# Kernel optimization log

Hardware: AMD Instinct MI355X
Metric: run time of the kernel (lower is better)

## Reference

```python
import jax, jax.numpy as jnp
import numpy as np

B, L, H = 32, 512, 1024
Q = 128
VA_H = 256

def setup_inputs() -> dict:
    key = jax.random.key(0)
    ks = jax.random.split(key, 12)
    hidden_states = jax.random.normal(ks[0], (B, L, H), dtype=jnp.float32)
    # Build valid inclusive spans: start in [2, L-16), length in [0, 8)
    asp_s = jax.random.randint(ks[1], (B, Q), 2, L - 16)
    asp_e = asp_s + jax.random.randint(ks[2], (B, Q), 0, 8)
    opi_s = jax.random.randint(ks[3], (B, Q), 2, L - 16)
    opi_e = opi_s + jax.random.randint(ks[4], (B, Q), 0, 8)
    null = jax.random.uniform(ks[5], (B, Q)) < 0.1
    asp_s = jnp.where(null, 0, asp_s)
    quad_spans = jnp.stack([asp_s, asp_e, opi_s, opi_e], axis=-1).astype(jnp.int64)
    quad_mask = (jax.random.uniform(ks[6], (B, Q)) > 0.3).astype(jnp.float32)
    # MLP params (torch Linear: y = x @ W.T + b), kaiming-ish scale
    def lin(k, out_d, in_d):
        return jax.random.normal(k, (out_d, in_d), dtype=jnp.float32) / np.sqrt(in_d)
    W1 = lin(ks[7], VA_H, 3 * H); b1 = jnp.zeros((VA_H,), jnp.float32)
    W2 = lin(ks[8], VA_H // 2, VA_H); b2 = jnp.zeros((VA_H // 2,), jnp.float32)
    W3 = lin(ks[9], 2, VA_H // 2); b3 = jnp.zeros((2,), jnp.float32)
    return {"hidden_states": hidden_states, "quad_spans": quad_spans,
            "quad_mask": quad_mask, "W1": W1, "b1": b1, "W2": W2, "b2": b2,
            "W3": W3, "b3": b3}

def _pool_spans(hidden_states, s, e):
    # hidden_states: [B,L,H]; s,e: [B,Q] inclusive indices
    pos = jnp.arange(hidden_states.shape[1])  # [L]
    valid = (s >= 2) & (e >= s)               # [B,Q]
    m = (pos[None, None, :] >= s[..., None]) & (pos[None, None, :] <= e[..., None])
    m = (m & valid[..., None]).astype(hidden_states.dtype)  # [B,Q,L]
    cnt = jnp.maximum(m.sum(-1, keepdims=True), 1.0)        # [B,Q,1]
    mean = jnp.einsum('bql,blh->bqh', m, hidden_states) / cnt
    sep = hidden_states[:, 1:2, :]                           # [B,1,H] fallback
    return jnp.where(valid[..., None], mean, sep)

def reference(hidden_states, quad_spans, quad_mask, W1, b1, W2, b2, W3, b3):
    h_asp = _pool_spans(hidden_states, quad_spans[..., 0], quad_spans[..., 1])
    h_opi = _pool_spans(hidden_states, quad_spans[..., 2], quad_spans[..., 3])
    h_pair = jnp.concatenate([h_asp, h_opi, h_asp * h_opi], axis=-1)  # [B,Q,3H]
    x = jax.nn.gelu(h_pair @ W1.T + b1, approximate=False)  # torch GELU = erf
    x = jax.nn.gelu(x @ W2.T + b2, approximate=False)
    va = jax.nn.sigmoid(x @ W3.T + b3) * 8.0 + 1.0          # [B,Q,2] in [1,9]
    # Invalid pairs stay zero, matching the torch loop's skipped entries
    return va * (quad_mask >= 0.5).astype(va.dtype)[..., None]
```

## Files before the change

kernel.cpp:

```cpp
#include <hip/hip_runtime.h>
#include <hip/hip_bf16.h>
#include <math.h>

typedef __bf16 bf16x8 __attribute__((ext_vector_type(8)));
typedef float f32x4 __attribute__((ext_vector_type(4)));

__device__ __forceinline__ unsigned short f2bf(float x) {
    union { float f; unsigned int u; } v; v.f = x;
    unsigned int r = v.u + 0x7fffu + ((v.u >> 16) & 1u);
    return (unsigned short)(r >> 16);
}
__device__ __forceinline__ float gelu_exact(float v) {
    return 0.5f * v * (1.0f + erff(v * 0.70710678118654752f));
}

template<int N>
__device__ __forceinline__ void pool_sum(const float4* __restrict__ base, int s, int tid, float4& out) {
    float4 v[N];
#pragma unroll
    for (int t = 0; t < N; ++t) v[t] = base[(s + t) * 256 + tid];
    float x = 0.f, y = 0.f, z = 0.f, w = 0.f;
#pragma unroll
    for (int t = 0; t < N; ++t) { x += v[t].x; y += v[t].y; z += v[t].z; w += v[t].w; }
    const float inv = 1.0f / (float)N;
    out.x = x * inv; out.y = y * inv; out.z = z * inv; out.w = w * inv;
}

__device__ __forceinline__ void pool_dispatch(const float4* __restrict__ base, int s, int len, int tid, float4& out) {
    switch (len) {
        case 1: pool_sum<1>(base, s, tid, out); break;
        case 2: pool_sum<2>(base, s, tid, out); break;
        case 3: pool_sum<3>(base, s, tid, out); break;
        case 4: pool_sum<4>(base, s, tid, out); break;
        case 5: pool_sum<5>(base, s, tid, out); break;
        case 6: pool_sum<6>(base, s, tid, out); break;
        case 7: pool_sum<7>(base, s, tid, out); break;
        default: pool_sum<8>(base, s, tid, out); break;
    }
}

__global__ __launch_bounds__(256) void prep_kernel(const float* __restrict__ hs,
                                                   const int* __restrict__ spans,
                                                   const float* __restrict__ W1,
                                                   const float* __restrict__ W2,
                                                   unsigned short* __restrict__ hp,
                                                   unsigned short* __restrict__ w1b,
                                                   unsigned short* __restrict__ w2b) {
    const int blk = blockIdx.x;
    const int tid = threadIdx.x;

    if (blk >= 4096) {
        if (blk < 4864) {
            const int i = (blk - 4096) * 256 + tid;
            float4 f = ((const float4*)W1)[i];
            ushort4 u;
            u.x = f2bf(f.x); u.y = f2bf(f.y); u.z = f2bf(f.z); u.w = f2bf(f.w);
            ((ushort4*)w1b)[i] = u;
        } else {
            const int i = (blk - 4864) * 256 + tid;
            float4 f = ((const float4*)W2)[i];
            ushort4 u;
            u.x = f2bf(f.x); u.y = f2bf(f.y); u.z = f2bf(f.z); u.w = f2bf(f.w);
            ((ushort4*)w2b)[i] = u;
        }
        return;
    }

    const int pair = blk;
    const int b = pair >> 7;

    const bool is64 = (spans[1] == 0);
    int s_a, e_a, s_o, e_o;
    if (is64) {
        s_a = spans[(pair * 4 + 0) * 2]; e_a = spans[(pair * 4 + 1) * 2];
        s_o = spans[(pair * 4 + 2) * 2]; e_o = spans[(pair * 4 + 3) * 2];
    } else {
        s_a = spans[pair * 4 + 0]; e_a = spans[pair * 4 + 1];
        s_o = spans[pair * 4 + 2]; e_o = spans[pair * 4 + 3];
    }

    if (!(s_a >= 2 && e_a >= s_a)) { s_a = 1; e_a = 1; }
    if (!(s_o >= 2 && e_o >= s_o)) { s_o = 1; e_o = 1; }
    const int lenA = e_a - s_a + 1;
    const int lenO = e_o - s_o + 1;

    const float4* base = (const float4*)hs + (size_t)b * 512 * 256;

    float4 A, O;
    pool_dispatch(base, s_a, lenA, tid, A);
    pool_dispatch(base, s_o, lenO, tid, O);

    unsigned short* row = hp + (size_t)pair * 3072;
    const int d = tid * 4;
    ushort4 pa, po, pp;
    pa.x = f2bf(A.x); pa.y = f2bf(A.y); pa.z = f2bf(A.z); pa.w = f2bf(A.w);
    po.x = f2bf(O.x); po.y = f2bf(O.y); po.z = f2bf(O.z); po.w = f2bf(O.w);
    pp.x = f2bf(A.x * O.x); pp.y = f2bf(A.y * O.y);
    pp.z = f2bf(A.z * O.z); pp.w = f2bf(A.w * O.w);
    *(ushort4*)(row + d) = pa;
    *(ushort4*)(row + 1024 + d) = po;
    *(ushort4*)(row + 2048 + d) = pp;
}

__global__ __launch_bounds__(256, 2) void gemm1_gelu(const unsigned short* __restrict__ A,
                                                     const unsigned short* __restrict__ Bw,
                                                     const float* __restrict__ b1,
                                                     unsigned short* __restrict__ x1) {
    __shared__ __align__(16) unsigned short As[2 * 32 * 192];
    __shared__ __align__(16) unsigned short Bs[2 * 64 * 192];

    const int tid = threadIdx.x;
    const int lane = tid & 63;
    const int wid = tid >> 6;
    const int quad = lane >> 4;
    const int l16 = lane & 15;

    const int id = blockIdx.x;
    const int xcd = id & 7;
    const int sub = id >> 3;
    const int m0 = (xcd * 16 + (sub >> 2)) * 32;
    const int n0 = (sub & 3) * 64;

    const unsigned short* Aptr[3];
#pragma unroll
    for (int p = 0; p < 3; ++p) {
        const int s = p * 256 + tid;
        const int row = s / 24;
        const int c = s - row * 24;
        const int lch = (c & 24) | ((c & 7) ^ (row & 7));
        Aptr[p] = A + (size_t)(m0 + row) * 3072 + lch * 8;
    }
    const unsigned short* Bptr[6];
#pragma unroll
    for (int p = 0; p < 6; ++p) {
        const int s = p * 256 + tid;
        const int row = s / 24;
        const int c = s - row * 24;
        const int lch = (c & 24) | ((c & 7) ^ (row & 7));
        Bptr[p] = Bw + (size_t)(n0 + row) * 3072 + lch * 8;
    }

    int aoff[2][6], boff[6];
#pragma unroll
    for (int h = 0; h < 6; ++h) {
        const int c = h * 4 + quad;
#pragma unroll
        for (int mh = 0; mh < 2; ++mh) {
            const int row = mh * 16 + l16;
            const int pc = (c & 24) | ((c & 7) ^ (row & 7));
            aoff[mh][h] = row * 192 + pc * 8;
        }
        const int brow = wid * 16 + l16;
        const int pcb = (c & 24) | ((c & 7) ^ (brow & 7));
        boff[h] = brow * 192 + pcb * 8;
    }

    f32x4 acc[2] = {};

#pragma unroll
    for (int p = 0; p < 3; ++p)
        __builtin_amdgcn_global_load_lds(
            (const __attribute__((address_space(1))) void*)Aptr[p],
            (__attribute__((address_space(3))) void*)(&As[(p * 256 + tid) * 8]), 16, 0, 0);
#pragma unroll
    for (int p = 0; p < 6; ++p)
        __builtin_amdgcn_global_load_lds(
            (const __attribute__((address_space(1))) void*)Bptr[p],
            (__attribute__((address_space(3))) void*)(&Bs[(p * 256 + tid) * 8]), 16, 0, 0);

    for (int it = 0; it < 16; ++it) {
        const int cur = it & 1;
        __syncthreads();
        if (it + 1 < 16) {
            const int nxt = cur ^ 1;
            const int kadv = (it + 1) * 192;
#pragma unroll
            for (int p = 0; p < 3; ++p)
                __builtin_amdgcn_global_load_lds(
                    (const __attribute__((address_space(1))) void*)(Aptr[p] + kadv),
                    (__attribute__((address_space(3))) void*)(&As[nxt * 6144 + (p * 256 + tid) * 8]), 16, 0, 0);
#pragma unroll
            for (int p = 0; p < 6; ++p)
                __builtin_amdgcn_global_load_lds(
                    (const __attribute__((address_space(1))) void*)(Bptr[p] + kadv),
                    (__attribute__((address_space(3))) void*)(&Bs[nxt * 12288 + (p * 256 + tid) * 8]), 16, 0, 0);
        }
#pragma unroll
        for (int h = 0; h < 6; ++h) {
            bf16x8 b = *(const bf16x8*)&Bs[cur * 12288 + boff[h]];
#pragma unroll
            for (int mh = 0; mh < 2; ++mh) {
                bf16x8 a = *(const bf16x8*)&As[cur * 6144 + aoff[mh][h]];
                acc[mh] = __builtin_amdgcn_mfma_f32_16x16x32_bf16(a, b, acc[mh], 0, 0, 0);
            }
        }
    }

    const int n = n0 + wid * 16 + l16;
    const float bn = b1[n];
#pragma unroll
    for (int mh = 0; mh < 2; ++mh) {
#pragma unroll
        for (int rr = 0; rr < 4; ++rr) {
            const int m = m0 + mh * 16 + quad * 4 + rr;
            x1[(size_t)m * 256 + n] = f2bf(gelu_exact(acc[mh][rr] + bn));
        }
    }
}

__global__ __launch_bounds__(256) void mlp2_head(const unsigned short* __restrict__ x1,
                                                 const unsigned short* __restrict__ w2b,
                                                 const float* __restrict__ b2,
                                                 const float* __restrict__ W3,
                                                 const float* __restrict__ b3,
                                                 const float* __restrict__ mask,
                                                 float* __restrict__ out) {
    __shared__ __align__(16) unsigned char smem[98304];
    unsigned short* Xs = (unsigned short*)smem;
    unsigned short* Ws = (unsigned short*)(smem + 16384);
    float*          X2 = (float*)(smem + 81920);

    const int tid = threadIdx.x;
    const int lane = tid & 63;
    const int wid = tid >> 6;
    const int quad = lane >> 4;
    const int l16 = lane & 15;
    const int wM = (wid >> 1) * 16;
    const int wN = (wid & 1) * 64;
    const int m0 = blockIdx.x * 32;

#pragma unroll
    for (int p = 0; p < 4; ++p) {
        const int s = p * 256 + tid;
        const int row = s >> 5;
        const int c = s & 31;
        const int lch = (c & 24) | ((c & 7) ^ (row & 7));
        __builtin_amdgcn_global_load_lds(
            (const __attribute__((address_space(1))) void*)(x1 + (size_t)(m0 + row) * 256 + lch * 8),
            (__attribute__((address_space(3))) void*)(&Xs[s * 8]), 16, 0, 0);
    }
#pragma unroll
    for (int p = 0; p < 16; ++p) {
        const int s = p * 256 + tid;
        const int row = s >> 5;
        const int c = s & 31;
        const int lch = (c & 24) | ((c & 7) ^ (row & 7));
        __builtin_amdgcn_global_load_lds(
            (const __attribute__((address_space(1))) void*)(w2b + (size_t)row * 256 + lch * 8),
            (__attribute__((address_space(3))) void*)(&Ws[s * 8]), 16, 0, 0);
    }
    __syncthreads();

    f32x4 acc[4] = {};
#pragma unroll
    for (int h = 0; h < 8; ++h) {
        const int c = h * 4 + quad;
        const int rowa = wM + l16;
        const int pca = (c & 24) | ((c & 7) ^ (rowa & 7));
        bf16x8 a = *(const bf16x8*)&Xs[rowa * 256 + pca * 8];
#pragma unroll
        for (int ni = 0; ni < 4; ++ni) {
            const int rowb = wN + ni * 16 + l16;
            const int pcb = (c & 24) | ((c & 7) ^ (rowb & 7));
            bf16x8 b = *(const bf16x8*)&Ws[rowb * 256 + pcb * 8];
            acc[ni] = __builtin_amdgcn_mfma_f32_16x16x32_bf16(a, b, acc[ni], 0, 0, 0);
        }
    }

#pragma unroll
    for (int ni = 0; ni < 4; ++ni) {
        const int n = wN + ni * 16 + l16;
        const float bn = b2[n];
#pragma unroll
        for (int rr = 0; rr < 4; ++rr) {
            const int m = wM + quad * 4 + rr;
            X2[m * 128 + n] = gelu_exact(acc[ni][rr] + bn);
        }
    }
    __syncthreads();

    const int p = tid >> 3;
    const int cc = (tid & 7) * 16;
    float a0 = 0.f, a1 = 0.f;
#pragma unroll
    for (int j = 0; j < 16; ++j) {
        const float xv = X2[p * 128 + cc + j];
        a0 += xv * W3[cc + j];
        a1 += xv * W3[128 + cc + j];
    }
    a0 += __shfl_xor(a0, 1); a0 += __shfl_xor(a0, 2); a0 += __shfl_xor(a0, 4);
    a1 += __shfl_xor(a1, 1); a1 += __shfl_xor(a1, 2); a1 += __shfl_xor(a1, 4);
    if ((tid & 7) == 0) {
        const int pair = m0 + p;
        const float mk = (mask[pair] >= 0.5f) ? 1.0f : 0.0f;
        out[pair * 2 + 0] = ((1.0f / (1.0f + expf(-(a0 + b3[0])))) * 8.0f + 1.0f) * mk;
        out[pair * 2 + 1] = ((1.0f / (1.0f + expf(-(a1 + b3[1])))) * 8.0f + 1.0f) * mk;
    }
}

extern "C" void kernel_launch(void* const* d_in, const int* in_sizes, int n_in,
                              void* d_out, int out_size, void* d_ws, size_t ws_size,
                              hipStream_t stream) {
    const float* hs   = (const float*)d_in[0];
    const int*   spans= (const int*)d_in[1];
    const float* mask = (const float*)d_in[2];
    const float* W1   = (const float*)d_in[3];
    const float* b1   = (const float*)d_in[4];
    const float* W2   = (const float*)d_in[5];
    const float* b2   = (const float*)d_in[6];
    const float* W3   = (const float*)d_in[7];
    const float* b3   = (const float*)d_in[8];
    float* out = (float*)d_out;

    unsigned short* hp  = (unsigned short*)d_ws;
    unsigned short* w1b = (unsigned short*)((char*)d_ws + 25165824);
    unsigned short* x1  = (unsigned short*)((char*)d_ws + 26738688);
    unsigned short* w2b = (unsigned short*)((char*)d_ws + 28835840);

    prep_kernel<<<dim3(4896), dim3(256), 0, stream>>>(hs, spans, W1, W2, hp, w1b, w2b);
    gemm1_gelu<<<dim3(512), dim3(256), 0, stream>>>(hp, w1b, b1, x1);
    mlp2_head<<<dim3(128), dim3(256), 0, stream>>>(x1, w2b, b2, W3, b3, mask, out);
}
```

Measured before the change: 145.3 us.

## Fuse prep, GEMM1 and MLP head into one cooperative persistent kernel

```diff
diff --git a/kernel.cpp b/kernel.cpp
--- a/kernel.cpp
+++ b/kernel.cpp
@@ -1,6 +1,9 @@
 #include <hip/hip_runtime.h>
+#include <hip/hip_cooperative_groups.h>
 #include <hip/hip_bf16.h>
 #include <math.h>
+
+namespace cg = cooperative_groups;
 
 typedef __bf16 bf16x8 __attribute__((ext_vector_type(8)));
 typedef float f32x4 __attribute__((ext_vector_type(4)));
@@ -25,7 +28,6 @@
     const float inv = 1.0f / (float)N;
     out.x = x * inv; out.y = y * inv; out.z = z * inv; out.w = w * inv;
 }
-
 __device__ __forceinline__ void pool_dispatch(const float4* __restrict__ base, int s, int len, int tid, float4& out) {
     switch (len) {
         case 1: pool_sum<1>(base, s, tid, out); break;
@@ -39,262 +41,248 @@
     }
 }
 
-__global__ __launch_bounds__(256) void prep_kernel(const float* __restrict__ hs,
-                                                   const int* __restrict__ spans,
-                                                   const float* __restrict__ W1,
-                                                   const float* __restrict__ W2,
-                                                   unsigned short* __restrict__ hp,
-                                                   unsigned short* __restrict__ w1b,
-                                                   unsigned short* __restrict__ w2b) {
-    const int blk = blockIdx.x;
+__global__ __launch_bounds__(256, 2) void fused_all(
+        const float* __restrict__ hs, const int* __restrict__ spans,
+        const float* __restrict__ W1, const float* __restrict__ b1,
+        const float* __restrict__ W2, const float* __restrict__ b2,
+        const float* __restrict__ W3, const float* __restrict__ b3,
+        const float* __restrict__ mask, float* __restrict__ out,
+        unsigned short* __restrict__ hp, unsigned short* __restrict__ w1b,
+        unsigned short* __restrict__ x1, unsigned short* __restrict__ w2b) {
+    __shared__ __align__(16) unsigned char smem[73728];
+    unsigned short* As = (unsigned short*)smem;
+    unsigned short* Bs = (unsigned short*)(smem + 24576);
+    unsigned short* Ws = (unsigned short*)smem;
+    float*      scratch = (float*)(smem + 65536);
+
     const int tid = threadIdx.x;
-
-    if (blk >= 4096) {
-        if (blk < 4864) {
-            const int i = (blk - 4096) * 256 + tid;
-            float4 f = ((const float4*)W1)[i];
-            ushort4 u;
-            u.x = f2bf(f.x); u.y = f2bf(f.y); u.z = f2bf(f.z); u.w = f2bf(f.w);
-            ((ushort4*)w1b)[i] = u;
-        } else {
-            const int i = (blk - 4864) * 256 + tid;
-            float4 f = ((const float4*)W2)[i];
-            ushort4 u;
-            u.x = f2bf(f.x); u.y = f2bf(f.y); u.z = f2bf(f.z); u.w = f2bf(f.w);
-            ((ushort4*)w2b)[i] = u;
-        }
-        return;
-    }
-
-    const int pair = blk;
-    const int b = pair >> 7;
-
-    const bool is64 = (spans[1] == 0);
-    int s_a, e_a, s_o, e_o;
-    if (is64) {
-        s_a = spans[(pair * 4 + 0) * 2]; e_a = spans[(pair * 4 + 1) * 2];
-        s_o = spans[(pair * 4 + 2) * 2]; e_o = spans[(pair * 4 + 3) * 2];
-    } else {
-        s_a = spans[pair * 4 + 0]; e_a = spans[pair * 4 + 1];
-        s_o = spans[pair * 4 + 2]; e_o = spans[pair * 4 + 3];
-    }
-
-    if (!(s_a >= 2 && e_a >= s_a)) { s_a = 1; e_a = 1; }
-    if (!(s_o >= 2 && e_o >= s_o)) { s_o = 1; e_o = 1; }
-    const int lenA = e_a - s_a + 1;
-    const int lenO = e_o - s_o + 1;
-
-    const float4* base = (const float4*)hs + (size_t)b * 512 * 256;
-
-    float4 A, O;
-    pool_dispatch(base, s_a, lenA, tid, A);
-    pool_dispatch(base, s_o, lenO, tid, O);
-
-    unsigned short* row = hp + (size_t)pair * 3072;
-    const int d = tid * 4;
-    ushort4 pa, po, pp;
-    pa.x = f2bf(A.x); pa.y = f2bf(A.y); pa.z = f2bf(A.z); pa.w = f2bf(A.w);
-    po.x = f2bf(O.x); po.y = f2bf(O.y); po.z = f2bf(O.z); po.w = f2bf(O.w);
-    pp.x = f2bf(A.x * O.x); pp.y = f2bf(A.y * O.y);
-    pp.z = f2bf(A.z * O.z); pp.w = f2bf(A.w * O.w);
-    *(ushort4*)(row + d) = pa;
-    *(ushort4*)(row + 1024 + d) = po;
-    *(ushort4*)(row + 2048 + d) = pp;
-}
-
-__global__ __launch_bounds__(256, 2) void gemm1_gelu(const unsigned short* __restrict__ A,
-                                                     const unsigned short* __restrict__ Bw,
-                                                     const float* __restrict__ b1,
-                                                     unsigned short* __restrict__ x1) {
-    __shared__ __align__(16) unsigned short As[2 * 32 * 192];
-    __shared__ __align__(16) unsigned short Bs[2 * 64 * 192];
-
-    const int tid = threadIdx.x;
+    const int id = blockIdx.x;
     const int lane = tid & 63;
     const int wid = tid >> 6;
     const int quad = lane >> 4;
     const int l16 = lane & 15;
 
-    const int id = blockIdx.x;
     const int xcd = id & 7;
     const int sub = id >> 3;
-    const int m0 = (xcd * 16 + (sub >> 2)) * 32;
-    const int n0 = (sub & 3) * 64;
-
-    const unsigned short* Aptr[3];
-#pragma unroll
-    for (int p = 0; p < 3; ++p) {
-        const int s = p * 256 + tid;
-        const int row = s / 24;
-        const int c = s - row * 24;
-        const int lch = (c & 24) | ((c & 7) ^ (row & 7));
-        Aptr[p] = A + (size_t)(m0 + row) * 3072 + lch * 8;
+    const int mp = xcd * 16 + (sub >> 2);
+    const int jj = sub & 3;
+    const int m0 = mp * 32;
+    const int n0 = jj * 64;
+
+    {
+        const bool is64 = (spans[1] == 0);
+        for (int pp = 0; pp < 8; ++pp) {
+            const int pair = m0 + jj * 8 + pp;
+            const int b = pair >> 7;
+            int s_a, e_a, s_o, e_o;
+            if (is64) {
+                s_a = spans[(pair * 4 + 0) * 2]; e_a = spans[(pair * 4 + 1) * 2];
+                s_o = spans[(pair * 4 + 2) * 2]; e_o = spans[(pair * 4 + 3) * 2];
+            } else {
+                s_a = spans[pair * 4 + 0]; e_a = spans[pair * 4 + 1];
+                s_o = spans[pair * 4 + 2]; e_o = spans[pair * 4 + 3];
+            }
+            if (!(s_a >= 2 && e_a >= s_a)) { s_a = 1; e_a = 1; }
+            if (!(s_o >= 2 && e_o >= s_o)) { s_o = 1; e_o = 1; }
+            const float4* base = (const float4*)hs + (size_t)b * 512 * 256;
+            float4 A, O;
+            pool_dispatch(base, s_a, e_a - s_a + 1, tid, A);
+            pool_dispatch(base, s_o, e_o - s_o + 1, tid, O);
+
+            unsigned short* row = hp + (size_t)pair * 3072;
+            const int d = tid * 4;
+            ushort4 pa, po, pq;
+            pa.x = f2bf(A.x); pa.y = f2bf(A.y); pa.z = f2bf(A.z); pa.w = f2bf(A.w);
+            po.x = f2bf(O.x); po.y = f2bf(O.y); po.z = f2bf(O.z); po.w = f2bf(O.w);
+            pq.x = f2bf(A.x * O.x); pq.y = f2bf(A.y * O.y);
+            pq.z = f2bf(A.z * O.z); pq.w = f2bf(A.w * O.w);
+            *(ushort4*)(row + d) = pa;
+            *(ushort4*)(row + 1024 + d) = po;
+            *(ushort4*)(row + 2048 + d) = pq;
+        }
+        const int g = id * 256 + tid;
+        {
+            float4 f = ((const float4*)W1)[g];
+            ushort4 u;
+            u.x = f2bf(f.x); u.y = f2bf(f.y); u.z = f2bf(f.z); u.w = f2bf(f.w);
+            ((ushort4*)w1b)[g] = u;
+            const int g2 = g + 131072;
+            if (g2 < 196608) {
+                float4 f2 = ((const float4*)W1)[g2];
+                ushort4 u2;
+                u2.x = f2bf(f2.x); u2.y = f2bf(f2.y); u2.z = f2bf(f2.z); u2.w = f2bf(f2.w);
+                ((ushort4*)w1b)[g2] = u2;
+            }
+        }
+        if (g < 8192) {
+            float4 f = ((const float4*)W2)[g];
+            ushort4 u;
+            u.x = f2bf(f.x); u.y = f2bf(f.y); u.z = f2bf(f.z); u.w = f2bf(f.w);
+            ((ushort4*)w2b)[g] = u;
+        }
     }
-    const unsigned short* Bptr[6];
-#pragma unroll
-    for (int p = 0; p < 6; ++p) {
-        const int s = p * 256 + tid;
-        const int row = s / 24;
-        const int c = s - row * 24;
-        const int lch = (c & 24) | ((c & 7) ^ (row & 7));
-        Bptr[p] = Bw + (size_t)(n0 + row) * 3072 + lch * 8;
+    __threadfence();
+    cg::this_grid().sync();
+
+    {
+        const unsigned short* Ap = hp;
+        const unsigned short* Bw = w1b;
+
+        const unsigned short* Aptr[3];
+#pragma unroll
+        for (int p = 0; p < 3; ++p) {
+            const int s = p * 256 + tid;
+            const int row = s / 24;
+            const int c = s - row * 24;
+            const int lch = (c & 24) | ((c & 7) ^ (row & 7));
+            Aptr[p] = Ap + (size_t)(m0 + row) * 3072 + lch * 8;
+        }
+        const unsigned short* Bptr[6];
+#pragma unroll
+        for (int p = 0; p < 6; ++p) {
+            const int s = p * 256 + tid;
+            const int row = s / 24;
+            const int c = s - row * 24;
+            const int lch = (c & 24) | ((c & 7) ^ (row & 7));
+            Bptr[p] = Bw + (size_t)(n0 + row) * 3072 + lch * 8;
+        }
+
+        int aoff[2][6], boff[6];
+#pragma unroll
+        for (int h = 0; h < 6; ++h) {
+            const int c = h * 4 + quad;
+#pragma unroll
+            for (int mh = 0; mh < 2; ++mh) {
+                const int row = mh * 16 + l16;
+                const int pc = (c & 24) | ((c & 7) ^ (row & 7));
+                aoff[mh][h] = row * 192 + pc * 8;
+            }
+            const int brow = wid * 16 + l16;
+            const int pcb = (c & 24) | ((c & 7) ^ (brow & 7));
+            boff[h] = brow * 192 + pcb * 8;
+        }
+
+        f32x4 acc[2] = {};
+
+#pragma unroll
+        for (int p = 0; p < 3; ++p)
+            __builtin_amdgcn_global_load_lds(
+                (const __attribute__((address_space(1))) void*)Aptr[p],
+                (__attribute__((address_space(3))) void*)(&As[(p * 256 + tid) * 8]), 16, 0, 0);
+#pragma unroll
+        for (int p = 0; p < 6; ++p)
+            __builtin_amdgcn_global_load_lds(
+                (const __attribute__((address_space(1))) void*)Bptr[p],
+                (__attribute__((address_space(3))) void*)(&Bs[(p * 256 + tid) * 8]), 16, 0, 0);
+
+        for (int it = 0; it < 16; ++it) {
+            const int cur = it & 1;
+            __syncthreads();
+            if (it + 1 < 16) {
+                const int nxt = cur ^ 1;
+                const int kadv = (it + 1) * 192;
+#pragma unroll
+                for (int p = 0; p < 3; ++p)
+                    __builtin_amdgcn_global_load_lds(
+                        (const __attribute__((address_space(1))) void*)(Aptr[p] + kadv),
+                        (__attribute__((address_space(3))) void*)(&As[nxt * 6144 + (p * 256 + tid) * 8]), 16, 0, 0);
+#pragma unroll
+                for (int p = 0; p < 6; ++p)
+                    __builtin_amdgcn_global_load_lds(
+                        (const __attribute__((address_space(1))) void*)(Bptr[p] + kadv),
+                        (__attribute__((address_space(3))) void*)(&Bs[nxt * 12288 + (p * 256 + tid) * 8]), 16, 0, 0);
+            }
+#pragma unroll
+            for (int h = 0; h < 6; ++h) {
+                bf16x8 bfr = *(const bf16x8*)&Bs[cur * 12288 + boff[h]];
+#pragma unroll
+                for (int mh = 0; mh < 2; ++mh) {
+                    bf16x8 afr = *(const bf16x8*)&As[cur * 6144 + aoff[mh][h]];
+                    acc[mh] = __builtin_amdgcn_mfma_f32_16x16x32_bf16(afr, bfr, acc[mh], 0, 0, 0);
+                }
+            }
+        }
+
+        const int n = n0 + wid * 16 + l16;
+        const float bn = b1[n];
+#pragma unroll
+        for (int mh = 0; mh < 2; ++mh) {
+#pragma unroll
+            for (int rr = 0; rr < 4; ++rr) {
+                const int m = m0 + mh * 16 + quad * 4 + rr;
+                x1[(size_t)m * 256 + n] = f2bf(gelu_exact(acc[mh][rr] + bn));
+            }
+        }
     }
-
-    int aoff[2][6], boff[6];
-#pragma unroll
-    for (int h = 0; h < 6; ++h) {
-        const int c = h * 4 + quad;
-#pragma unroll
-        for (int mh = 0; mh < 2; ++mh) {
-            const int row = mh * 16 + l16;
-            const int pc = (c & 24) | ((c & 7) ^ (row & 7));
-            aoff[mh][h] = row * 192 + pc * 8;
-        }
-        const int brow = wid * 16 + l16;
-        const int pcb = (c & 24) | ((c & 7) ^ (brow & 7));
-        boff[h] = brow * 192 + pcb * 8;
-    }
-
-    f32x4 acc[2] = {};
-
-#pragma unroll
-    for (int p = 0; p < 3; ++p)
-        __builtin_amdgcn_global_load_lds(
-            (const __attribute__((address_space(1))) void*)Aptr[p],
-            (__attribute__((address_space(3))) void*)(&As[(p * 256 + tid) * 8]), 16, 0, 0);
-#pragma unroll
-    for (int p = 0; p < 6; ++p)
-        __builtin_amdgcn_global_load_lds(
-            (const __attribute__((address_space(1))) void*)Bptr[p],
-            (__attribute__((address_space(3))) void*)(&Bs[(p * 256 + tid) * 8]), 16, 0, 0);
-
-    for (int it = 0; it < 16; ++it) {
-        const int cur = it & 1;
+    __threadfence();
+    cg::this_grid().sync();
+
+    if (id >= 128) return;
+    {
+        const int m0c = id * 32;
+        const int wM = (wid >> 1) * 16;
+        const int wN = (wid & 1) * 64;
+        const int half = wid & 1;
+
+#pragma unroll
+        for (int p = 0; p < 16; ++p) {
+            const int s = p * 256 + tid;
+            const int row = s >> 5;
+            const int c = s & 31;
+            const int lch = (c & 24) | ((c & 7) ^ (row & 7));
+            __builtin_amdgcn_global_load_lds(
+                (const __attribute__((address_space(1))) void*)(w2b + (size_t)row * 256 + lch * 8),
+                (__attribute__((address_space(3))) void*)(&Ws[s * 8]), 16, 0, 0);
+        }
         __syncthreads();
-        if (it + 1 < 16) {
-            const int nxt = cur ^ 1;
-            const int kadv = (it + 1) * 192;
-#pragma unroll
-            for (int p = 0; p < 3; ++p)
-                __builtin_amdgcn_global_load_lds(
-                    (const __attribute__((address_space(1))) void*)(Aptr[p] + kadv),
-                    (__attribute__((address_space(3))) void*)(&As[nxt * 6144 + (p * 256 + tid) * 8]), 16, 0, 0);
-#pragma unroll
-            for (int p = 0; p < 6; ++p)
-                __builtin_amdgcn_global_load_lds(
-                    (const __attribute__((address_space(1))) void*)(Bptr[p] + kadv),
-                    (__attribute__((address_space(3))) void*)(&Bs[nxt * 12288 + (p * 256 + tid) * 8]), 16, 0, 0);
-        }
-#pragma unroll
-        for (int h = 0; h < 6; ++h) {
-            bf16x8 b = *(const bf16x8*)&Bs[cur * 12288 + boff[h]];
-#pragma unroll
-            for (int mh = 0; mh < 2; ++mh) {
-                bf16x8 a = *(const bf16x8*)&As[cur * 6144 + aoff[mh][h]];
-                acc[mh] = __builtin_amdgcn_mfma_f32_16x16x32_bf16(a, b, acc[mh], 0, 0, 0);
-            }
-        }
-    }
-
-    const int n = n0 + wid * 16 + l16;
-    const float bn = b1[n];
-#pragma unroll
-    for (int mh = 0; mh < 2; ++mh) {
+
+        f32x4 acc2[4] = {};
+        const unsigned short* arow = x1 + (size_t)(m0c + wM + l16) * 256;
+#pragma unroll
+        for (int h = 0; h < 8; ++h) {
+            bf16x8 afr = *(const bf16x8*)(arow + h * 32 + quad * 8);
+#pragma unroll
+            for (int ni = 0; ni < 4; ++ni) {
+                const int rowb = wN + ni * 16 + l16;
+                const int c = h * 4 + quad;
+                const int pcb = (c & 24) | ((c & 7) ^ (rowb & 7));
+                bf16x8 bfr = *(const bf16x8*)&Ws[rowb * 256 + pcb * 8];
+                acc2[ni] = __builtin_amdgcn_mfma_f32_16x16x32_bf16(afr, bfr, acc2[ni], 0, 0, 0);
+            }
+        }
+
+        float b2v[4], w30[4], w31[4];
+#pragma unroll
+        for (int ni = 0; ni < 4; ++ni) {
+            const int col = wN + ni * 16 + l16;
+            b2v[ni] = b2[col]; w30[ni] = W3[col]; w31[ni] = W3[128 + col];
+        }
 #pragma unroll
         for (int rr = 0; rr < 4; ++rr) {
-            const int m = m0 + mh * 16 + quad * 4 + rr;
-            x1[(size_t)m * 256 + n] = f2bf(gelu_exact(acc[mh][rr] + bn));
-        }
-    }
-}
-
-__global__ __launch_bounds__(256) void mlp2_head(const unsigned short* __restrict__ x1,
-                                                 const unsigned short* __restrict__ w2b,
-                                                 const float* __restrict__ b2,
-                                                 const float* __restrict__ W3,
-                                                 const float* __restrict__ b3,
-                                                 const float* __restrict__ mask,
-                                                 float* __restrict__ out) {
-    __shared__ __align__(16) unsigned char smem[98304];
-    unsigned short* Xs = (unsigned short*)smem;
-    unsigned short* Ws = (unsigned short*)(smem + 16384);
-    float*          X2 = (float*)(smem + 81920);
-
-    const int tid = threadIdx.x;
-    const int lane = tid & 63;
-    const int wid = tid >> 6;
-    const int quad = lane >> 4;
-    const int l16 = lane & 15;
-    const int wM = (wid >> 1) * 16;
-    const int wN = (wid & 1) * 64;
-    const int m0 = blockIdx.x * 32;
-
-#pragma unroll
-    for (int p = 0; p < 4; ++p) {
-        const int s = p * 256 + tid;
-        const int row = s >> 5;
-        const int c = s & 31;
-        const int lch = (c & 24) | ((c & 7) ^ (row & 7));
-        __builtin_amdgcn_global_load_lds(
-            (const __attribute__((address_space(1))) void*)(x1 + (size_t)(m0 + row) * 256 + lch * 8),
-            (__attribute__((address_space(3))) void*)(&Xs[s * 8]), 16, 0, 0);
-    }
-#pragma unroll
-    for (int p = 0; p < 16; ++p) {
-        const int s = p * 256 + tid;
-        const int row = s >> 5;
-        const int c = s & 31;
-        const int lch = (c & 24) | ((c & 7) ^ (row & 7));
-        __builtin_amdgcn_global_load_lds(
-            (const __attribute__((address_space(1))) void*)(w2b + (size_t)row * 256 + lch * 8),
-            (__attribute__((address_space(3))) void*)(&Ws[s * 8]), 16, 0, 0);
-    }
-    __syncthreads();
-
-    f32x4 acc[4] = {};
-#pragma unroll
-    for (int h = 0; h < 8; ++h) {
-        const int c = h * 4 + quad;
-        const int rowa = wM + l16;
-        const int pca = (c & 24) | ((c & 7) ^ (rowa & 7));
-        bf16x8 a = *(const bf16x8*)&Xs[rowa * 256 + pca * 8];
-#pragma unroll
-        for (int ni = 0; ni < 4; ++ni) {
-            const int rowb = wN + ni * 16 + l16;
-            const int pcb = (c & 24) | ((c & 7) ^ (rowb & 7));
-            bf16x8 b = *(const bf16x8*)&Ws[rowb * 256 + pcb * 8];
-            acc[ni] = __builtin_amdgcn_mfma_f32_16x16x32_bf16(a, b, acc[ni], 0, 0, 0);
-        }
-    }
-
-#pragma unroll
-    for (int ni = 0; ni < 4; ++ni) {
-        const int n = wN + ni * 16 + l16;
-        const float bn = b2[n];
-#pragma unroll
-        for (int rr = 0; rr < 4; ++rr) {
-            const int m = wM + quad * 4 + rr;
-            X2[m * 128 + n] = gelu_exact(acc[ni][rr] + bn);
-        }
-    }
-    __syncthreads();
-
-    const int p = tid >> 3;
-    const int cc = (tid & 7) * 16;
-    float a0 = 0.f, a1 = 0.f;
-#pragma unroll
-    for (int j = 0; j < 16; ++j) {
-        const float xv = X2[p * 128 + cc + j];
-        a0 += xv * W3[cc + j];
-        a1 += xv * W3[128 + cc + j];
-    }
-    a0 += __shfl_xor(a0, 1); a0 += __shfl_xor(a0, 2); a0 += __shfl_xor(a0, 4);
-    a1 += __shfl_xor(a1, 1); a1 += __shfl_xor(a1, 2); a1 += __shfl_xor(a1, 4);
-    if ((tid & 7) == 0) {
-        const int pair = m0 + p;
-        const float mk = (mask[pair] >= 0.5f) ? 1.0f : 0.0f;
-        out[pair * 2 + 0] = ((1.0f / (1.0f + expf(-(a0 + b3[0])))) * 8.0f + 1.0f) * mk;
-        out[pair * 2 + 1] = ((1.0f / (1.0f + expf(-(a1 + b3[1])))) * 8.0f + 1.0f) * mk;
+            float t0 = 0.f, t1 = 0.f;
+#pragma unroll
+            for (int ni = 0; ni < 4; ++ni) {
+                const float xv = gelu_exact(acc2[ni][rr] + b2v[ni]);
+                t0 += xv * w30[ni]; t1 += xv * w31[ni];
+            }
+            t0 += __shfl_xor(t0, 1); t0 += __shfl_xor(t0, 2);
+            t0 += __shfl_xor(t0, 4); t0 += __shfl_xor(t0, 8);
+            t1 += __shfl_xor(t1, 1); t1 += __shfl_xor(t1, 2);
+            t1 += __shfl_xor(t1, 4); t1 += __shfl_xor(t1, 8);
+            if (l16 == 0) {
+                const int pb = wM + quad * 4 + rr;
+                scratch[(half * 32 + pb) * 2 + 0] = t0;
+                scratch[(half * 32 + pb) * 2 + 1] = t1;
+            }
+        }
+        __syncthreads();
+        if (tid < 64) {
+            const int pb = tid >> 1, o = tid & 1;
+            const float v = scratch[pb * 2 + o] + scratch[(32 + pb) * 2 + o];
+            const int pair = m0c + pb;
+            const float mk = (mask[pair] >= 0.5f) ? 1.0f : 0.0f;
+            out[pair * 2 + o] = ((1.0f / (1.0f + expf(-(v + b3[o])))) * 8.0f + 1.0f) * mk;
+        }
     }
 }
 
@@ -317,7 +305,10 @@
     unsigned short* x1  = (unsigned short*)((char*)d_ws + 26738688);
     unsigned short* w2b = (unsigned short*)((char*)d_ws + 28835840);
 
-    prep_kernel<<<dim3(4896), dim3(256), 0, stream>>>(hs, spans, W1, W2, hp, w1b, w2b);
-    gemm1_gelu<<<dim3(512), dim3(256), 0, stream>>>(hp, w1b, b1, x1);
-    mlp2_head<<<dim3(128), dim3(256), 0, stream>>>(x1, w2b, b2, W3, b3, mask, out);
-}
+    void* args[] = { (void*)&hs, (void*)&spans, (void*)&W1, (void*)&b1,
+                     (void*)&W2, (void*)&b2, (void*)&W3, (void*)&b3,
+                     (void*)&mask, (void*)&out,
+                     (void*)&hp, (void*)&w1b, (void*)&x1, (void*)&w2b };
+    hipLaunchCooperativeKernel((const void*)fused_all, dim3(512), dim3(256),
+                               args, 0, stream);
+}
```

Measured after the change: 375.3 us. 158% more time.
